# Performance work log

Hardware: AMD Instinct MI355X
Metric: run time of the kernel (lower is better)

The kernel has to match this reference:

```python
import jax, jax.numpy as jnp
import numpy as np

T, B, E, H = 2048, 4, 1024, 16
EH = E // H  # 64


def setup_inputs() -> dict:
    rng = jax.random.key(0)
    ks = jax.random.split(rng, 8)
    s = 0.02  # weight init scale to keep softmax logits reasonable
    return {
        "query": jax.random.normal(ks[0], (T, B, E), jnp.float32),
        "key": jax.random.normal(ks[1], (T, B, E), jnp.float32),
        "value": jax.random.normal(ks[2], (T, B, E), jnp.float32),
        "mask": jax.random.uniform(ks[3], (T, T), jnp.float32),
        "w_qkv": jax.random.normal(ks[4], (3 * E, E), jnp.float32) * s,
        "b_qkv": jax.random.normal(ks[5], (3 * E,), jnp.float32) * s,
        "w_out": jax.random.normal(ks[6], (E, E), jnp.float32) * s,
        "b_out": jax.random.normal(ks[7], (E,), jnp.float32) * s,
    }


def reference(query, key, value, mask, w_qkv, b_qkv, w_out, b_out):
    # query/key/value: [T, B, E] (sequence-first, as in the torch module)
    t, b, e = query.shape
    eh = e // H
    wq, wk, wv = jnp.split(w_qkv, 3, axis=0)  # each [E, E]
    bq, bk, bv = jnp.split(b_qkv, 3, axis=0)

    def proj_heads(x, w, bias):
        y = x @ w.T + bias                    # [T, B, E]
        # [T,B,H,Eh] -> [B,H,T,Eh]  (matches unflatten/transpose/permute chain)
        return y.reshape(t, b, H, eh).transpose(1, 2, 0, 3)

    q = proj_heads(query, wq, bq)             # [B, H, T, Eh]
    k = proj_heads(key, wk, bk)
    v = proj_heads(value, wv, bv)

    scale = 1.0 / np.sqrt(eh).astype(np.float32)
    scores = jnp.einsum('bhqd,bhkd->bhqk', q, k) * scale   # [B,H,T,T]
    scores = scores * mask[None, None, :, :]               # multiplicative mask
    # is_causal=False, attn_mask=None -> attn_bias is zeros (skip identity add)
    attn = jax.nn.softmax(scores, axis=-1)
    # dropout=0.0 -> identity
    ctx = jnp.einsum('bhqk,bhkd->bhqd', attn, v)           # [B,H,T,Eh]
    ctx = ctx.transpose(0, 2, 1, 3).reshape(b, t, e)       # [B,T,E]
    out = ctx @ w_out.T + b_out                            # [B,T,E]
    return out.transpose(1, 0, 2)                          # [T,B,E]
```

## Files before the change

### kernel.cpp

```cpp
#include <hip/hip_runtime.h>
#include <hip/hip_bf16.h>
#include <stdint.h>

#define T_DIM 2048
#define B_DIM 4
#define E_DIM 1024
#define H_DIM 16
#define EHD 64
#define L2E 1.4426950408889634f
#define QSCALE (0.125f * L2E)
#define FMAXC 12.0f

typedef __attribute__((ext_vector_type(8))) short bf16x8;
typedef __attribute__((ext_vector_type(4))) float f32x4;
typedef __attribute__((ext_vector_type(2))) float f32x2;
typedef __attribute__((ext_vector_type(2))) unsigned u32x2;

__device__ __forceinline__ unsigned short f2bf(float x) {
  unsigned int u = __builtin_bit_cast(unsigned int, x);
  u += 0x7fffu + ((u >> 16) & 1u);
  return (unsigned short)(u >> 16);
}

__device__ __forceinline__ unsigned pkbf(float a, float b) {
  return (unsigned)f2bf(a) | ((unsigned)f2bf(b) << 16);
}

__device__ __forceinline__ unsigned pk_trunc(float a, float b) {
  return (__builtin_bit_cast(unsigned, a) >> 16) |
         (__builtin_bit_cast(unsigned, b) & 0xffff0000u);
}

__device__ __forceinline__ f32x2 bfpair(unsigned lo, unsigned hi_w) {
  u32x2 u = {lo << 16, hi_w & 0xffff0000u};
  return __builtin_bit_cast(f32x2, u);
}

__device__ __forceinline__ void gload16(const void* g, void* l) {
  __builtin_amdgcn_global_load_lds(
      (const __attribute__((address_space(1))) void*)g,
      (__attribute__((address_space(3))) void*)l, 16, 0, 0);
}

__global__ __launch_bounds__(256) void cvt_fused(
    const float4* __restrict__ q, const float4* __restrict__ k,
    const float4* __restrict__ v, const float4* __restrict__ wqkv,
    const float4* __restrict__ wout, uint2* __restrict__ xq,
    uint2* __restrict__ xk, uint2* __restrict__ xv, uint2* __restrict__ wq,
    uint2* __restrict__ wo) {
  int i = blockIdx.x * 256 + threadIdx.x;
  const int stride = gridDim.x * 256;
  for (; i < 7340032; i += stride) {
    const float4* s;
    uint2* d;
    int j;
    if (i < 2097152) { s = q; d = xq; j = i; }
    else if (i < 4194304) { s = k; d = xk; j = i - 2097152; }
    else if (i < 6291456) { s = v; d = xv; j = i - 4194304; }
    else if (i < 7077888) { s = wqkv; d = wq; j = i - 6291456; }
    else { s = wout; d = wo; j = i - 7077888; }
    const float4 f = s[j];
    uint2 o;
    o.x = pkbf(f.x, f.y);
    o.y = pkbf(f.z, f.w);
    d[j] = o;
  }
}

__global__ __launch_bounds__(256) void mask_perm(const float* __restrict__ mask,
                                                 uint4* __restrict__ out) {
  const int c = blockIdx.x * 256 + threadIdx.x;
  const int lane = c & 63;
  const int g = (c >> 6) & 1;
  const int wave = (c >> 7) & 3;
  const int h = (c >> 9) & 1;
  const int t = (c >> 10) & 31;
  const int qblk = c >> 15;
  const int lrow = lane & 15, lgrp = lane >> 4;
  const int qq = qblk * 128 + g * 64 + wave * 16 + lrow;
  const int k0 = t * 64 + h * 32 + lgrp * 4;
  const float4 f0 = *(const float4*)(mask + (size_t)qq * T_DIM + k0);
  const float4 f1 = *(const float4*)(mask + (size_t)qq * T_DIM + k0 + 16);
  uint4 o;
  o.x = pkbf(f0.x, f0.y);
  o.y = pkbf(f0.z, f0.w);
  o.z = pkbf(f1.x, f1.y);
  o.w = pkbf(f1.z, f1.w);
  out[c] = o;
}

template <int MODE>
__global__ __launch_bounds__(256) void gemm_kernel(
    const unsigned short* __restrict__ Abase,
    const unsigned short* __restrict__ Bt,
    const float* __restrict__ bias,
    void* __restrict__ outv, int K) {
  __shared__ alignas(16) short As[128 * 32];
  __shared__ alignas(16) short Bs[128 * 32];
  const int tid = threadIdx.x;
  const int lane = tid & 63, wave = tid >> 6;
  const int m0 = blockIdx.x * 128, n0 = blockIdx.y * 128;
  const int wr = wave >> 1, wc = wave & 1;
  const int lrow = lane & 15, lgrp = lane >> 4;

  const unsigned short* A = Abase;
  if (MODE == 0) A += (size_t)(n0 >> 10) * (8192u * 1024u);

  f32x4 acc[4][4];
#pragma unroll
  for (int m = 0; m < 4; ++m)
#pragma unroll
    for (int n = 0; n < 4; ++n) acc[m][n] = (f32x4){0.f, 0.f, 0.f, 0.f};

  const int srow = wave * 16 + (lane >> 2);
  const int scol = (lane & 3) * 8;
  short* lA0 = As + wave * 16 * 32;
  short* lA1 = As + (64 + wave * 16) * 32;
  short* lB0 = Bs + wave * 16 * 32;
  short* lB1 = Bs + (64 + wave * 16) * 32;

  for (int k0 = 0; k0 < K; k0 += 32) {
    const unsigned short* ga = A + (size_t)(m0 + srow) * K + k0 + scol;
    const unsigned short* gb = Bt + (size_t)(n0 + srow) * K + k0 + scol;
    gload16(ga, lA0);
    gload16(ga + (size_t)64 * K, lA1);
    gload16(gb, lB0);
    gload16(gb + (size_t)64 * K, lB1);
    __syncthreads();
    const short* pa = As + (wr * 64 + lrow) * 32 + lgrp * 8;
    const short* pb = Bs + (wc * 64 + lrow) * 32 + lgrp * 8;
    bf16x8 a[4], b[4];
#pragma unroll
    for (int m = 0; m < 4; ++m) a[m] = *(const bf16x8*)(pa + m * 512);
#pragma unroll
    for (int n = 0; n < 4; ++n) b[n] = *(const bf16x8*)(pb + n * 512);
#pragma unroll
    for (int m = 0; m < 4; ++m)
#pragma unroll
      for (int n = 0; n < 4; ++n)
        acc[m][n] = __builtin_amdgcn_mfma_f32_16x16x32_bf16(a[m], b[n], acc[m][n], 0, 0, 0);
    __syncthreads();
  }

#pragma unroll
  for (int n = 0; n < 4; ++n) {
    const int gn = n0 + wc * 64 + n * 16 + lrow;
    const float bv = bias[gn];
    if (MODE == 0) {
      unsigned short* out = (unsigned short*)outv;
      const int which = gn >> 10;
      const float qsc = (which == 0) ? QSCALE : 1.0f;
      const int e = gn & 1023;
      const int hh = e >> 6, dd = e & 63;
#pragma unroll
      for (int m = 0; m < 4; ++m)
#pragma unroll
        for (int r = 0; r < 4; ++r) {
          const int gm = m0 + wr * 64 + m * 16 + lgrp * 4 + r;
          const int t = gm >> 2, bb = gm & 3;
          const unsigned short val = f2bf((acc[m][n][r] + bv) * qsc);
          if (which == 2) {
            out[((size_t)(2 * B_DIM * H_DIM) + bb * H_DIM + hh) * (T_DIM * EHD) +
                (size_t)(t >> 6) * 4096 + dd * 64 + (t & 63)] = val;
          } else {
            out[((size_t)which * B_DIM * H_DIM + bb * H_DIM + hh) * (T_DIM * EHD) +
                (size_t)t * EHD + dd] = val;
          }
        }
    } else {
      float* out = (float*)outv;
#pragma unroll
      for (int m = 0; m < 4; ++m)
#pragma unroll
        for (int r = 0; r < 4; ++r) {
          const int gm = m0 + wr * 64 + m * 16 + lgrp * 4 + r;
          const int bb = gm >> 11, t = gm & 2047;
          out[((size_t)t * B_DIM + bb) * E_DIM + gn] = acc[m][n][r] + bv;
        }
    }
  }
}

__global__ __launch_bounds__(256, 2) void attn_kernel(
    const unsigned short* __restrict__ Qm, const unsigned short* __restrict__ Km,
    const unsigned short* __restrict__ Vtm, const unsigned short* __restrict__ Mb,
    unsigned short* __restrict__ ctx) {
  __shared__ alignas(16) short Ks[2][4096];
  __shared__ alignas(16) short Vs[2][4096];
  __shared__ alignas(16) short Ml[2][8192];
  __shared__ alignas(16) short Pl[4][2][1024];
  const int tid = threadIdx.x, lane = tid & 63, wave = tid >> 6;
  const int lrow = lane & 15, lgrp = lane >> 4;
  const int bh = blockIdx.y, b = bh >> 4, h = bh & 15;
  const int q0 = blockIdx.x * 128;

  const size_t base = (size_t)bh * (T_DIM * EHD);
  const unsigned short* mbase = Mb + (size_t)blockIdx.x * 262144;

  bf16x8 qf0[2], qf1[2];
  int qrow[2];
#pragma unroll
  for (int g = 0; g < 2; ++g) {
    qrow[g] = q0 + g * 64 + wave * 16 + lrow;
    const unsigned short* qp = Qm + base + (size_t)qrow[g] * EHD + lgrp * 8;
    qf0[g] = *(const bf16x8*)qp;
    qf1[g] = *(const bf16x8*)(qp + 32);
  }

  f32x4 oacc[2][4];
#pragma unroll
  for (int g = 0; g < 2; ++g)
#pragma unroll
    for (int n = 0; n < 4; ++n) oacc[g][n] = (f32x4){0.f, 0.f, 0.f, 0.f};
  f32x2 racc[2] = {(f32x2){0.f, 0.f}, (f32x2){0.f, 0.f}};

  const int rr = lane >> 3;
  const int cs = (((lane & 7) ^ rr) * 8);
  const int r0w = wave * 8;
  const int rx = (lrow & 7) * 8;
  const int c0 = (lgrp * 8) ^ rx;

#define STAGE(bufi, T)                                                          \
  {                                                                             \
    const int kv0 = (T) * 64;                                                   \
    _Pragma("unroll") for (int i = 0; i < 2; ++i) {                             \
      const int r0 = i * 32 + r0w;                                              \
      gload16(Km + base + (size_t)(kv0 + r0 + rr) * EHD + cs,                   \
              &Ks[bufi][r0 * 64]);                                              \
      gload16(Vtm + base + (size_t)kv0 * EHD + (r0 + rr) * 64 + cs,             \
              &Vs[bufi][r0 * 64]);                                              \
    }                                                                           \
    _Pragma("unroll") for (int h2 = 0; h2 < 2; ++h2) {                          \
      _Pragma("unroll") for (int p = 0; p < 2; ++p) {                           \
        const int sl = (h2 * 4 + wave) * 2 + p;                                 \
        gload16(mbase + (size_t)(T) * 8192 + sl * 512 + lane * 8,               \
                &Ml[bufi][sl * 512]);                                           \
      }                                                                         \
    }                                                                           \
  }

  short* plw0 = &Pl[wave][0][lrow * 64];
  short* plw1 = &Pl[wave][1][lrow * 64];

#define ATTN_ITER(CUR, DO_PRE, TN)                                              \
  {                                                                             \
    if (DO_PRE) {                                                               \
      STAGE((CUR) ^ 1, TN);                                                     \
      __builtin_amdgcn_sched_barrier(0);                                        \
    }                                                                           \
    const short* kb = Ks[CUR];                                                  \
    const short* vb = Vs[CUR];                                                  \
    const short* mlb = Ml[CUR];                                                 \
    float sv[2][4][4];                                                          \
    __builtin_amdgcn_s_setprio(1);                                              \
    _Pragma("unroll") for (int n = 0; n < 4; ++n) {                             \
      const short* kp = kb + (n * 16 + lrow) * 64;                              \
      const bf16x8 kf0 = *(const bf16x8*)(kp + c0);                             \
      const bf16x8 kf1 = *(const bf16x8*)(kp + (c0 ^ 32));                      \
      f32x4 s0 = (f32x4){0.f, 0.f, 0.f, 0.f}, s1 = s0;                          \
      s0 = __builtin_amdgcn_mfma_f32_16x16x32_bf16(kf0, qf0[0], s0, 0, 0, 0);   \
      s0 = __builtin_amdgcn_mfma_f32_16x16x32_bf16(kf1, qf1[0], s0, 0, 0, 0);   \
      s1 = __builtin_amdgcn_mfma_f32_16x16x32_bf16(kf0, qf0[1], s1, 0, 0, 0);   \
      s1 = __builtin_amdgcn_mfma_f32_16x16x32_bf16(kf1, qf1[1], s1, 0, 0, 0);   \
      _Pragma("unroll") for (int r = 0; r < 4; ++r) {                           \
        sv[0][n][r] = s0[r];                                                    \
        sv[1][n][r] = s1[r];                                                    \
      }                                                                         \
    }                                                                           \
    __builtin_amdgcn_s_setprio(0);                                              \
    _Pragma("unroll") for (int g = 0; g < 2; ++g) {                             \
      short* plw = g ? plw1 : plw0;                                             \
      const uint4 m01 =                                                         \
          *(const uint4*)(mlb + (wave * 2 + g) * 512 + lane * 8);               \
      const uint4 m23 =                                                         \
          *(const uint4*)(mlb + ((4 + wave) * 2 + g) * 512 + lane * 8);         \
      const unsigned mwx[4] = {m01.x, m01.z, m23.x, m23.z};                     \
      const unsigned mwy[4] = {m01.y, m01.w, m23.y, m23.w};                     \
      _Pragma("unroll") for (int n = 0; n < 4; ++n) {                           \
        const f32x2 s01 = {sv[g][n][0], sv[g][n][1]};                           \
        const f32x2 s23 = {sv[g][n][2], sv[g][n][3]};                           \
        const f32x2 m0v = bfpair(mwx[n], mwx[n]);                               \
        const f32x2 m1v = bfpair(mwy[n], mwy[n]);                               \
        const f32x2 t01 = __builtin_elementwise_fma(                            \
            s01, m0v, (f32x2){-FMAXC, -FMAXC});                                 \
        const f32x2 t23 = __builtin_elementwise_fma(                            \
            s23, m1v, (f32x2){-FMAXC, -FMAXC});                                 \
        const float p0 = __builtin_amdgcn_exp2f(t01.x);                         \
        const float p1 = __builtin_amdgcn_exp2f(t01.y);                         \
        const float p2 = __builtin_amdgcn_exp2f(t23.x);                         \
        const float p3 = __builtin_amdgcn_exp2f(t23.y);                         \
        racc[g] += (f32x2){p0, p1} + (f32x2){p2, p3};                           \
        uint2 w;                                                                \
        w.x = pk_trunc(p0, p1);                                                 \
        w.y = pk_trunc(p2, p3);                                                 \
        *(uint2*)(plw + ((n * 16 + lgrp * 4) ^ rx)) = w;                        \
      }                                                                         \
    }                                                                           \
    __builtin_amdgcn_s_setprio(1);                                              \
    _Pragma("unroll") for (int kc = 0; kc < 2; ++kc) {                          \
      const int pc = ((kc * 32) + lgrp * 8) ^ rx;                               \
      const bf16x8 pB0 = *(const bf16x8*)(plw0 + pc);                           \
      const bf16x8 pB1 = *(const bf16x8*)(plw1 + pc);                           \
      _Pragma("unroll") for (int n = 0; n < 4; ++n) {                           \
        const bf16x8 vf = *(const bf16x8*)(vb + (n * 16 + lrow) * 64 + pc);     \
        oacc[0][n] = __builtin_amdgcn_mfma_f32_16x16x32_bf16(vf, pB0, oacc[0][n], 0, 0, 0); \
        oacc[1][n] = __builtin_amdgcn_mfma_f32_16x16x32_bf16(vf, pB1, oacc[1][n], 0, 0, 0); \
      }                                                                         \
    }                                                                           \
    __builtin_amdgcn_s_setprio(0);                                              \
  }

#define WAITBAR                                                                 \
  asm volatile("s_waitcnt vmcnt(0)" ::: "memory");                              \
  __builtin_amdgcn_sched_barrier(0);                                            \
  __builtin_amdgcn_s_barrier();                                                 \
  __builtin_amdgcn_sched_barrier(0);

  STAGE(0, 0);
  WAITBAR

  for (int tt = 0; tt < 15; ++tt) {
    ATTN_ITER(0, 1, 2 * tt + 1);
    WAITBAR
    ATTN_ITER(1, 1, 2 * tt + 2);
    WAITBAR
  }
  ATTN_ITER(0, 1, 31);
  WAITBAR
  ATTN_ITER(1, 0, 0);

#undef ATTN_ITER
#undef WAITBAR
#undef STAGE

#pragma unroll
  for (int g = 0; g < 2; ++g) {
    float lr = racc[g].x + racc[g].y;
    lr += __shfl_xor(lr, 16);
    lr += __shfl_xor(lr, 32);
    const float inv = 1.f / lr;
    unsigned short* cp =
        ctx + ((size_t)b * T_DIM + qrow[g]) * E_DIM + h * EHD + lgrp * 4;
#pragma unroll
    for (int n = 0; n < 4; ++n) {
      uint2 w;
      w.x = pkbf(oacc[g][n][0] * inv, oacc[g][n][1] * inv);
      w.y = pkbf(oacc[g][n][2] * inv, oacc[g][n][3] * inv);
      *(uint2*)(cp + n * 16) = w;
    }
  }
}

extern "C" void kernel_launch(void* const* d_in, const int* in_sizes, int n_in,
                              void* d_out, int out_size, void* d_ws, size_t ws_size,
                              hipStream_t stream) {
  const float* q    = (const float*)d_in[0];
  const float* k    = (const float*)d_in[1];
  const float* v    = (const float*)d_in[2];
  const float* mask = (const float*)d_in[3];
  const float* wqkv = (const float*)d_in[4];
  const float* bqkv = (const float*)d_in[5];
  const float* wout = (const float*)d_in[6];
  const float* bout = (const float*)d_in[7];

  char* ws = (char*)d_ws;
  unsigned short* Xb   = (unsigned short*)(ws);
  unsigned short* Wqb  = (unsigned short*)(ws + 50331648);
  unsigned short* Wob  = (unsigned short*)(ws + 56623104);
  unsigned short* QKVb = (unsigned short*)(ws + 58720256);
  unsigned short* CTXb = (unsigned short*)(ws);
  unsigned short* Mb   = (unsigned short*)(ws + 16777216);

  cvt_fused<<<2048, 256, 0, stream>>>(
      (const float4*)q, (const float4*)k, (const float4*)v,
      (const float4*)wqkv, (const float4*)wout, (uint2*)Xb,
      (uint2*)(Xb + 8388608), (uint2*)(Xb + 16777216), (uint2*)Wqb,
      (uint2*)Wob);

  gemm_kernel<0><<<dim3(64, 24), 256, 0, stream>>>(Xb, Wqb, bqkv, QKVb, 1024);
  mask_perm<<<2048, 256, 0, stream>>>(mask, (uint4*)Mb);
  attn_kernel<<<dim3(16, 64), 256, 0, stream>>>(QKVb, QKVb + 8388608,
                                                QKVb + 16777216, Mb, CTXb);
  gemm_kernel<1><<<dim3(64, 8), 256, 0, stream>>>(CTXb, Wob, bout, d_out, 1024);
}
```

Baseline: 269.3 us.

## Switch attention to 32x32x16 MFMA with register-resident P via permlane32 swap

Rewrites the attention inner loop to use 32x32x16 bf16 MFMAs with one 32-row query tile per wave. The softmax probabilities stay in registers and are reshuffled into the B-operand layout with v_permlane32_swap instead of a round trip through LDS. The QKV projection epilogue and the mask permutation kernel now write K, V and the mask in pre-swizzled fragment layouts, so every LDS fragment load becomes one contiguous 16-byte read per lane. This removes the P scratch buffer and its LDS traffic, and uses fewer, larger MFMA instructions. In exchange it needs more accumulator registers per wave, and the GEMM now does scattered stores to build the new layouts.

```diff
diff --git a/kernel.cpp b/kernel.cpp
--- a/kernel.cpp
+++ b/kernel.cpp
@@ -13,8 +13,10 @@
 
 typedef __attribute__((ext_vector_type(8))) short bf16x8;
 typedef __attribute__((ext_vector_type(4))) float f32x4;
+typedef __attribute__((ext_vector_type(16))) float f32x16;
 typedef __attribute__((ext_vector_type(2))) float f32x2;
 typedef __attribute__((ext_vector_type(2))) unsigned u32x2;
+typedef __attribute__((ext_vector_type(4))) unsigned u32x4;
 
 __device__ __forceinline__ unsigned short f2bf(float x) {
   unsigned int u = __builtin_bit_cast(unsigned int, x);
@@ -31,8 +33,8 @@
          (__builtin_bit_cast(unsigned, b) & 0xffff0000u);
 }
 
-__device__ __forceinline__ f32x2 bfpair(unsigned lo, unsigned hi_w) {
-  u32x2 u = {lo << 16, hi_w & 0xffff0000u};
+__device__ __forceinline__ f32x2 bfpair1(unsigned w) {
+  u32x2 u = {w << 16, w & 0xffff0000u};
   return __builtin_bit_cast(f32x2, u);
 }
 
@@ -71,16 +73,16 @@
                                                  uint4* __restrict__ out) {
   const int c = blockIdx.x * 256 + threadIdx.x;
   const int lane = c & 63;
-  const int g = (c >> 6) & 1;
-  const int wave = (c >> 7) & 3;
-  const int h = (c >> 9) & 1;
+  const int half = (c >> 6) & 1;
+  const int kb = (c >> 7) & 1;
+  const int wave = (c >> 8) & 3;
   const int t = (c >> 10) & 31;
   const int qblk = c >> 15;
-  const int lrow = lane & 15, lgrp = lane >> 4;
-  const int qq = qblk * 128 + g * 64 + wave * 16 + lrow;
-  const int k0 = t * 64 + h * 32 + lgrp * 4;
-  const float4 f0 = *(const float4*)(mask + (size_t)qq * T_DIM + k0);
-  const float4 f1 = *(const float4*)(mask + (size_t)qq * T_DIM + k0 + 16);
+  const int hi = lane >> 5;
+  const int qq = qblk * 128 + wave * 32 + (lane & 31);
+  const int kbase = t * 64 + kb * 32 + half * 16 + hi * 4;
+  const float4 f0 = *(const float4*)(mask + (size_t)qq * T_DIM + kbase);
+  const float4 f1 = *(const float4*)(mask + (size_t)qq * T_DIM + kbase + 8);
   uint4 o;
   o.x = pkbf(f0.x, f0.y);
   o.y = pkbf(f0.z, f0.w);
@@ -159,12 +161,17 @@
           const int gm = m0 + wr * 64 + m * 16 + lgrp * 4 + r;
           const int t = gm >> 2, bb = gm & 3;
           const unsigned short val = f2bf((acc[m][n][r] + bv) * qsc);
-          if (which == 2) {
-            out[((size_t)(2 * B_DIM * H_DIM) + bb * H_DIM + hh) * (T_DIM * EHD) +
-                (size_t)(t >> 6) * 4096 + dd * 64 + (t & 63)] = val;
+          const size_t rbase = ((size_t)which * 64 + bb * 16 + hh) * 131072;
+          if (which == 0) {
+            out[rbase + (size_t)t * 64 + dd] = val;
+          } else if (which == 1) {
+            out[rbase + (t >> 6) * 4096 +
+                (((t >> 5) & 1) * 4 + (dd >> 4)) * 512 +
+                ((((dd >> 3) & 1) << 5) + (t & 31)) * 8 + (dd & 7)] = val;
           } else {
-            out[((size_t)which * B_DIM * H_DIM + bb * H_DIM + hh) * (T_DIM * EHD) +
-                (size_t)t * EHD + dd] = val;
+            out[rbase + (t >> 6) * 4096 +
+                ((dd >> 5) * 4 + ((t >> 4) & 3)) * 512 +
+                ((((t >> 3) & 1) << 5) + (dd & 31)) * 8 + (t & 7)] = val;
           }
         }
     } else {
@@ -182,65 +189,80 @@
 }
 
 __global__ __launch_bounds__(256, 2) void attn_kernel(
-    const unsigned short* __restrict__ Qm, const unsigned short* __restrict__ Km,
-    const unsigned short* __restrict__ Vtm, const unsigned short* __restrict__ Mb,
+    const unsigned short* __restrict__ Qm, const unsigned short* __restrict__ KPg,
+    const unsigned short* __restrict__ VPg, const unsigned short* __restrict__ Mb,
     unsigned short* __restrict__ ctx) {
   __shared__ alignas(16) short Ks[2][4096];
   __shared__ alignas(16) short Vs[2][4096];
   __shared__ alignas(16) short Ml[2][8192];
-  __shared__ alignas(16) short Pl[4][2][1024];
   const int tid = threadIdx.x, lane = tid & 63, wave = tid >> 6;
-  const int lrow = lane & 15, lgrp = lane >> 4;
+  const int ql = lane & 31, hi = lane >> 5;
   const int bh = blockIdx.y, b = bh >> 4, h = bh & 15;
   const int q0 = blockIdx.x * 128;
+  const int qrow = q0 + wave * 32 + ql;
 
   const size_t base = (size_t)bh * (T_DIM * EHD);
   const unsigned short* mbase = Mb + (size_t)blockIdx.x * 262144;
 
-  bf16x8 qf0[2], qf1[2];
-  int qrow[2];
-#pragma unroll
-  for (int g = 0; g < 2; ++g) {
-    qrow[g] = q0 + g * 64 + wave * 16 + lrow;
-    const unsigned short* qp = Qm + base + (size_t)qrow[g] * EHD + lgrp * 8;
-    qf0[g] = *(const bf16x8*)qp;
-    qf1[g] = *(const bf16x8*)(qp + 32);
-  }
-
-  f32x4 oacc[2][4];
-#pragma unroll
-  for (int g = 0; g < 2; ++g)
-#pragma unroll
-    for (int n = 0; n < 4; ++n) oacc[g][n] = (f32x4){0.f, 0.f, 0.f, 0.f};
-  f32x2 racc[2] = {(f32x2){0.f, 0.f}, (f32x2){0.f, 0.f}};
-
-  const int rr = lane >> 3;
-  const int cs = (((lane & 7) ^ rr) * 8);
-  const int r0w = wave * 8;
-  const int rx = (lrow & 7) * 8;
-  const int c0 = (lgrp * 8) ^ rx;
-
-#define STAGE(bufi, T)                                                          \
+  bf16x8 qf[4];
+#pragma unroll
+  for (int i = 0; i < 4; ++i)
+    qf[i] = *(const bf16x8*)(Qm + base + (size_t)qrow * 64 + i * 16 + hi * 8);
+
+  f32x16 accO0 = {0.f, 0.f, 0.f, 0.f, 0.f, 0.f, 0.f, 0.f,
+                  0.f, 0.f, 0.f, 0.f, 0.f, 0.f, 0.f, 0.f};
+  f32x16 accO1 = accO0;
+  float racc = 0.f;
+
+#define STAGE(bufi, T_)                                                         \
   {                                                                             \
-    const int kv0 = (T) * 64;                                                   \
-    _Pragma("unroll") for (int i = 0; i < 2; ++i) {                             \
-      const int r0 = i * 32 + r0w;                                              \
-      gload16(Km + base + (size_t)(kv0 + r0 + rr) * EHD + cs,                   \
-              &Ks[bufi][r0 * 64]);                                              \
-      gload16(Vtm + base + (size_t)kv0 * EHD + (r0 + rr) * 64 + cs,             \
-              &Vs[bufi][r0 * 64]);                                              \
-    }                                                                           \
-    _Pragma("unroll") for (int h2 = 0; h2 < 2; ++h2) {                          \
-      _Pragma("unroll") for (int p = 0; p < 2; ++p) {                           \
-        const int sl = (h2 * 4 + wave) * 2 + p;                                 \
-        gload16(mbase + (size_t)(T) * 8192 + sl * 512 + lane * 8,               \
-                &Ml[bufi][sl * 512]);                                           \
-      }                                                                         \
-    }                                                                           \
-  }
-
-  short* plw0 = &Pl[wave][0][lrow * 64];
-  short* plw1 = &Pl[wave][1][lrow * 64];
+    _Pragma("unroll") for (int s2 = 0; s2 < 2; ++s2) {                          \
+      const int s = wave * 2 + s2;                                              \
+      gload16(KPg + base + (size_t)(T_) * 4096 + s * 512 + lane * 8,            \
+              &Ks[bufi][s * 512]);                                              \
+      gload16(VPg + base + (size_t)(T_) * 4096 + s * 512 + lane * 8,            \
+              &Vs[bufi][s * 512]);                                              \
+    }                                                                           \
+    _Pragma("unroll") for (int u = 0; u < 4; ++u) {                             \
+      const int s = wave * 4 + u;                                               \
+      gload16(mbase + (size_t)(T_) * 8192 + s * 512 + lane * 8,                 \
+              &Ml[bufi][s * 512]);                                              \
+    }                                                                           \
+  }
+
+#define SOFTW(ACC, KB, HALF, W, MW)                                             \
+  {                                                                             \
+    const f32x2 mm = bfpair1(MW);                                               \
+    const f32x2 sv = {ACC[HALF * 8 + 2 * W], ACC[HALF * 8 + 2 * W + 1]};        \
+    const f32x2 tt =                                                            \
+        __builtin_elementwise_fma(sv, mm, (f32x2){-FMAXC, -FMAXC});             \
+    const float p0 = __builtin_amdgcn_exp2f(tt.x);                              \
+    const float p1 = __builtin_amdgcn_exp2f(tt.y);                              \
+    racc += p0 + p1;                                                            \
+    wk[KB][HALF * 4 + W] = pk_trunc(p0, p1);                                    \
+  }
+
+#define SOFTHALF(ACC, KB, HALF, MU)                                             \
+  SOFTW(ACC, KB, HALF, 0, (MU).x)                                               \
+  SOFTW(ACC, KB, HALF, 1, (MU).y)                                               \
+  SOFTW(ACC, KB, HALF, 2, (MU).z)                                               \
+  SOFTW(ACC, KB, HALF, 3, (MU).w)
+
+#define PVCHUNK(KB, HF)                                                         \
+  {                                                                             \
+    unsigned a0 = wk[KB][HF * 4 + 0], a1 = wk[KB][HF * 4 + 1];                  \
+    unsigned a2 = wk[KB][HF * 4 + 2], a3 = wk[KB][HF * 4 + 3];                  \
+    asm("v_permlane32_swap_b32 %0, %1" : "+v"(a0), "+v"(a2));                   \
+    asm("v_permlane32_swap_b32 %0, %1" : "+v"(a1), "+v"(a3));                   \
+    const u32x4 pw = {a0, a1, a2, a3};                                          \
+    const bf16x8 pa = __builtin_bit_cast(bf16x8, pw);                           \
+    const bf16x8 vf0 =                                                          \
+        *(const bf16x8*)(vb + (0 + (KB)*2 + (HF)) * 512 + lane * 8);            \
+    const bf16x8 vf1 =                                                          \
+        *(const bf16x8*)(vb + (4 + (KB)*2 + (HF)) * 512 + lane * 8);            \
+    accO0 = __builtin_amdgcn_mfma_f32_32x32x16_bf16(vf0, pa, accO0, 0, 0, 0);   \
+    accO1 = __builtin_amdgcn_mfma_f32_32x32x16_bf16(vf1, pa, accO1, 0, 0, 0);   \
+  }
 
 #define ATTN_ITER(CUR, DO_PRE, TN)                                              \
   {                                                                             \
@@ -248,65 +270,38 @@
       STAGE((CUR) ^ 1, TN);                                                     \
       __builtin_amdgcn_sched_barrier(0);                                        \
     }                                                                           \
-    const short* kb = Ks[CUR];                                                  \
+    const short* kbl = Ks[CUR];                                                 \
     const short* vb = Vs[CUR];                                                  \
-    const short* mlb = Ml[CUR];                                                 \
-    float sv[2][4][4];                                                          \
+    const short* ml = Ml[CUR];                                                  \
+    f32x16 accS0 = {0.f, 0.f, 0.f, 0.f, 0.f, 0.f, 0.f, 0.f,                     \
+                    0.f, 0.f, 0.f, 0.f, 0.f, 0.f, 0.f, 0.f};                    \
+    f32x16 accS1 = accS0;                                                       \
     __builtin_amdgcn_s_setprio(1);                                              \
-    _Pragma("unroll") for (int n = 0; n < 4; ++n) {                             \
-      const short* kp = kb + (n * 16 + lrow) * 64;                              \
-      const bf16x8 kf0 = *(const bf16x8*)(kp + c0);                             \
-      const bf16x8 kf1 = *(const bf16x8*)(kp + (c0 ^ 32));                      \
-      f32x4 s0 = (f32x4){0.f, 0.f, 0.f, 0.f}, s1 = s0;                          \
-      s0 = __builtin_amdgcn_mfma_f32_16x16x32_bf16(kf0, qf0[0], s0, 0, 0, 0);   \
-      s0 = __builtin_amdgcn_mfma_f32_16x16x32_bf16(kf1, qf1[0], s0, 0, 0, 0);   \
-      s1 = __builtin_amdgcn_mfma_f32_16x16x32_bf16(kf0, qf0[1], s1, 0, 0, 0);   \
-      s1 = __builtin_amdgcn_mfma_f32_16x16x32_bf16(kf1, qf1[1], s1, 0, 0, 0);   \
-      _Pragma("unroll") for (int r = 0; r < 4; ++r) {                           \
-        sv[0][n][r] = s0[r];                                                    \
-        sv[1][n][r] = s1[r];                                                    \
-      }                                                                         \
+    _Pragma("unroll") for (int i = 0; i < 4; ++i) {                             \
+      const bf16x8 kf = *(const bf16x8*)(kbl + i * 512 + lane * 8);             \
+      accS0 = __builtin_amdgcn_mfma_f32_32x32x16_bf16(kf, qf[i], accS0, 0, 0, 0); \
+    }                                                                           \
+    _Pragma("unroll") for (int i = 0; i < 4; ++i) {                             \
+      const bf16x8 kf = *(const bf16x8*)(kbl + (4 + i) * 512 + lane * 8);       \
+      accS1 = __builtin_amdgcn_mfma_f32_32x32x16_bf16(kf, qf[i], accS1, 0, 0, 0); \
     }                                                                           \
     __builtin_amdgcn_s_setprio(0);                                              \
-    _Pragma("unroll") for (int g = 0; g < 2; ++g) {                             \
-      short* plw = g ? plw1 : plw0;                                             \
-      const uint4 m01 =                                                         \
-          *(const uint4*)(mlb + (wave * 2 + g) * 512 + lane * 8);               \
-      const uint4 m23 =                                                         \
-          *(const uint4*)(mlb + ((4 + wave) * 2 + g) * 512 + lane * 8);         \
-      const unsigned mwx[4] = {m01.x, m01.z, m23.x, m23.z};                     \
-      const unsigned mwy[4] = {m01.y, m01.w, m23.y, m23.w};                     \
-      _Pragma("unroll") for (int n = 0; n < 4; ++n) {                           \
-        const f32x2 s01 = {sv[g][n][0], sv[g][n][1]};                           \
-        const f32x2 s23 = {sv[g][n][2], sv[g][n][3]};                           \
-        const f32x2 m0v = bfpair(mwx[n], mwx[n]);                               \
-        const f32x2 m1v = bfpair(mwy[n], mwy[n]);                               \
-        const f32x2 t01 = __builtin_elementwise_fma(                            \
-            s01, m0v, (f32x2){-FMAXC, -FMAXC});                                 \
-        const f32x2 t23 = __builtin_elementwise_fma(                            \
-            s23, m1v, (f32x2){-FMAXC, -FMAXC});                                 \
-        const float p0 = __builtin_amdgcn_exp2f(t01.x);                         \
-        const float p1 = __builtin_amdgcn_exp2f(t01.y);                         \
-        const float p2 = __builtin_amdgcn_exp2f(t23.x);                         \
-        const float p3 = __builtin_amdgcn_exp2f(t23.y);                         \
-        racc[g] += (f32x2){p0, p1} + (f32x2){p2, p3};                           \
-        uint2 w;                                                                \
-        w.x = pk_trunc(p0, p1);                                                 \
-        w.y = pk_trunc(p2, p3);                                                 \
-        *(uint2*)(plw + ((n * 16 + lgrp * 4) ^ rx)) = w;                        \
-      }                                                                         \
+    unsigned wk[2][8];                                                          \
+    {                                                                           \
+      const uint4 m0 = *(const uint4*)(ml + (wave * 4 + 0) * 512 + lane * 8);   \
+      const uint4 m1 = *(const uint4*)(ml + (wave * 4 + 1) * 512 + lane * 8);   \
+      SOFTHALF(accS0, 0, 0, m0)                                                 \
+      SOFTHALF(accS0, 0, 1, m1)                                                 \
+      const uint4 m2 = *(const uint4*)(ml + (wave * 4 + 2) * 512 + lane * 8);   \
+      const uint4 m3 = *(const uint4*)(ml + (wave * 4 + 3) * 512 + lane * 8);   \
+      SOFTHALF(accS1, 1, 0, m2)                                                 \
+      SOFTHALF(accS1, 1, 1, m3)                                                 \
     }                                                                           \
     __builtin_amdgcn_s_setprio(1);                                              \
-    _Pragma("unroll") for (int kc = 0; kc < 2; ++kc) {                          \
-      const int pc = ((kc * 32) + lgrp * 8) ^ rx;                               \
-      const bf16x8 pB0 = *(const bf16x8*)(plw0 + pc);                           \
-      const bf16x8 pB1 = *(const bf16x8*)(plw1 + pc);                           \
-      _Pragma("unroll") for (int n = 0; n < 4; ++n) {                           \
-        const bf16x8 vf = *(const bf16x8*)(vb + (n * 16 + lrow) * 64 + pc);     \
-        oacc[0][n] = __builtin_amdgcn_mfma_f32_16x16x32_bf16(vf, pB0, oacc[0][n], 0, 0, 0); \
-        oacc[1][n] = __builtin_amdgcn_mfma_f32_16x16x32_bf16(vf, pB1, oacc[1][n], 0, 0, 0); \
-      }                                                                         \
-    }                                                                           \
+    PVCHUNK(0, 0)                                                               \
+    PVCHUNK(0, 1)                                                               \
+    PVCHUNK(1, 0)                                                               \
+    PVCHUNK(1, 1)                                                               \
     __builtin_amdgcn_s_setprio(0);                                              \
   }
 
@@ -332,23 +327,24 @@
 #undef ATTN_ITER
 #undef WAITBAR
 #undef STAGE
-
-#pragma unroll
-  for (int g = 0; g < 2; ++g) {
-    float lr = racc[g].x + racc[g].y;
-    lr += __shfl_xor(lr, 16);
-    lr += __shfl_xor(lr, 32);
-    const float inv = 1.f / lr;
-    unsigned short* cp =
-        ctx + ((size_t)b * T_DIM + qrow[g]) * E_DIM + h * EHD + lgrp * 4;
-#pragma unroll
-    for (int n = 0; n < 4; ++n) {
-      uint2 w;
-      w.x = pkbf(oacc[g][n][0] * inv, oacc[g][n][1] * inv);
-      w.y = pkbf(oacc[g][n][2] * inv, oacc[g][n][3] * inv);
-      *(uint2*)(cp + n * 16) = w;
-    }
-  }
+#undef PVCHUNK
+#undef SOFTHALF
+#undef SOFTW
+
+  racc += __shfl_xor(racc, 32);
+  const float inv = 1.f / racc;
+  unsigned short* cp =
+      ctx + ((size_t)b * T_DIM + qrow) * E_DIM + h * 64 + hi * 4;
+#define EPI(ACC, DBLK)                                                          \
+  _Pragma("unroll") for (int rg = 0; rg < 4; ++rg) {                            \
+    uint2 w;                                                                    \
+    w.x = pkbf(ACC[rg * 4 + 0] * inv, ACC[rg * 4 + 1] * inv);                   \
+    w.y = pkbf(ACC[rg * 4 + 2] * inv, ACC[rg * 4 + 3] * inv);                   \
+    *(uint2*)(cp + (DBLK)*32 + rg * 8) = w;                                     \
+  }
+  EPI(accO0, 0)
+  EPI(accO1, 1)
+#undef EPI
 }
 
 extern "C" void kernel_launch(void* const* d_in, const int* in_sizes, int n_in,
```

Result: faster. 255.3 us (-5.2%).
